# Performance work log

Measured on AMD Instinct MI355X. Metric: run time of the kernel, lower is better.

Reference implementation:

```python
import jax, jax.numpy as jnp
import numpy as np

N = 50000   # nodes
E = 1600000 # edges
D = 128     # feature dim (in = hidden = 128)


def setup_inputs() -> dict:
    key = jax.random.key(0)
    k1, k2, k3, k4 = jax.random.split(key, 4)
    scale = 1.0 / np.sqrt(D)
    return {
        "x": jax.random.normal(k1, (N, D), jnp.float32),
        "edge_index": jax.random.randint(k2, (2, E), 0, N, dtype=jnp.int32),
        "W0": jax.random.normal(k3, (D, D), jnp.float32) * scale,
        "b0": jnp.zeros((D,), jnp.float32),
        "W1": jax.random.normal(k4, (D, D), jnp.float32) * scale,
        "b1": jnp.zeros((D,), jnp.float32),
    }


def _gcn_norm(edge_index, num_nodes):
    # Add self-loops, compute symmetric normalization D^-1/2 A_hat D^-1/2.
    loop = jnp.arange(num_nodes, dtype=edge_index.dtype)
    src = jnp.concatenate([edge_index[0], loop])
    dst = jnp.concatenate([edge_index[1], loop])
    deg = jax.ops.segment_sum(jnp.ones_like(dst, jnp.float32), dst,
                              num_segments=num_nodes)
    dinv = jnp.where(deg > 0, jax.lax.rsqrt(deg), 0.0)
    norm = dinv[dst] * dinv[src]  # [E+N]
    return src, dst, norm


def _gcn_layer(x, src, dst, norm, W, b, num_nodes):
    h = x @ W                                  # [N, D]
    msg = h[src] * norm[:, None]               # gather + scale  [E+N, D]
    out = jax.ops.segment_sum(msg, dst, num_segments=num_nodes)  # scatter-add
    return out + b


def reference(x, edge_index, W0, b0, W1, b1):
    num_nodes = x.shape[0]
    src, dst, norm = _gcn_norm(edge_index, num_nodes)
    # forward loops over the first k=2 convs, ReLU after each (as in source)
    x = jax.nn.relu(_gcn_layer(x, src, dst, norm, W0, b0, num_nodes))
    x = jax.nn.relu(_gcn_layer(x, src, dst, norm, W1, b1, num_nodes))
    return x
```

## Files before the change

kernel.cpp:

```cpp
#include <hip/hip_runtime.h>
#include <hip/hip_bf16.h>

#define D 128
#define CHUNK 8192
#define SPAN_CAP 768


typedef __attribute__((ext_vector_type(8))) short short8;
typedef __attribute__((ext_vector_type(4))) float floatx4;

static __device__ inline unsigned int f2bf(float f) {
    unsigned int u = __float_as_uint(f);
    return (u + 0x7FFFu + ((u >> 16) & 1u)) >> 16;
}
static __device__ inline float bflo(unsigned int u) { return __uint_as_float(u << 16); }
static __device__ inline float bfhi(unsigned int u) { return __uint_as_float(u & 0xFFFF0000u); }

__global__ __launch_bounds__(256) void k01_swz_hist(const float* __restrict__ W0,
                                                    const float* __restrict__ W1,
                                                    short8* __restrict__ whi0, short8* __restrict__ wlo0,
                                                    short8* __restrict__ whi1, short8* __restrict__ wlo1,
                                                    const int* __restrict__ dst,
                                                    int* __restrict__ blockhist, int E_) {
    __shared__ int h[256];
    const int tid = threadIdx.x;
    if (blockIdx.x < 16) {
        int gid = blockIdx.x * 256 + tid;
        const float* W = (gid < 2048) ? W0 : W1;
        short8* whi = (gid < 2048) ? whi0 : whi1;
        short8* wlo = (gid < 2048) ? wlo0 : wlo1;
        int t2 = gid & 2047;
        int t = t2 >> 8, q = (t2 >> 6) & 3, lane = t2 & 63;
        short8 hi, lo;
        #pragma unroll
        for (int j = 0; j < 8; ++j) {
            int k = q * 32 + (lane >> 4) * 8 + j;
            int n = t * 16 + (lane & 15);
            float w = W[k * D + n];
            unsigned int hh = f2bf(w);
            hi[j] = (short)hh;
            lo[j] = (short)f2bf(w - __uint_as_float(hh << 16));
        }
        whi[t2] = hi;
        wlo[t2] = lo;
    } else {
        const int b = blockIdx.x - 16;
        h[tid] = 0;
        __syncthreads();
        const int e0 = b * CHUNK;
        const int e1 = min(E_, e0 + CHUNK);
        for (int e = e0 + tid; e < e1; e += 256)
            atomicAdd(&h[dst[e] >> 8], 1);
        __syncthreads();
        blockhist[b * 256 + tid] = h[tid];
    }
}

__global__ __launch_bounds__(256) void k23_scan_scatter(const int* __restrict__ blockhist,
                                                        const int* __restrict__ dst,
                                                        const int* __restrict__ src,
                                                        int* __restrict__ bucket_offs,
                                                        unsigned int* __restrict__ buf,
                                                        int NB, int NBUK, int E_) {
    __shared__ int s[256];
    __shared__ int c[256];
    const int myb = blockIdx.x, tid = threadIdx.x;
    int total = 0, prefix = 0;
    #pragma unroll 4
    for (int b2 = 0; b2 < NB; ++b2) {
        int t = blockhist[b2 * 256 + tid];
        total += t;
        prefix += (b2 < myb) ? t : 0;
    }
    s[tid] = total;
    __syncthreads();
    #pragma unroll
    for (int off = 1; off < 256; off <<= 1) {
        int x = (tid >= off) ? s[tid - off] : 0;
        __syncthreads();
        s[tid] += x;
        __syncthreads();
    }
    int bstart = s[tid] - total;
    if (myb == 0) {
        if (tid < NBUK) bucket_offs[tid] = bstart;
        if (tid == 0) bucket_offs[NBUK] = E_;
    }
    c[tid] = bstart + prefix;
    __syncthreads();

    const int e0 = myb * CHUNK;
    const int e1 = min(E_, e0 + CHUNK);
    for (int e = e0 + tid; e < e1; e += 256) {
        int v = dst[e];
        int sdx = src[e];
        int pos = atomicAdd(&c[v >> 8], 1);
        buf[pos] = (unsigned int)sdx | ((unsigned int)(v & 255) << 16);
    }
}

__global__ __launch_bounds__(256) void k4_bucket(const unsigned int* __restrict__ buf,
                                                 const int* __restrict__ bucket_offs,
                                                 int* __restrict__ offs,
                                                 float* __restrict__ dinv,
                                                 int* __restrict__ col, int N_, int E_) {
    __shared__ int h[256];
    __shared__ int s[256];
    __shared__ int c[256];
    const int beta = blockIdx.x, tid = threadIdx.x;
    const int start = bucket_offs[beta];
    const int end   = bucket_offs[beta + 1];

    h[tid] = 0;
    __syncthreads();
    for (int e = start + tid; e < end; e += 256)
        atomicAdd(&h[(buf[e] >> 16) & 255], 1);
    __syncthreads();

    int deg = h[tid];
    s[tid] = deg;
    __syncthreads();
    #pragma unroll
    for (int off = 1; off < 256; off <<= 1) {
        int x = (tid >= off) ? s[tid - off] : 0;
        __syncthreads();
        s[tid] += x;
        __syncthreads();
    }
    int excl = s[tid] - deg;

    int v0 = beta * 256 + tid;
    if (v0 < N_) {
        offs[v0] = start + excl;
        dinv[v0] = rsqrtf((float)(deg + 1));
    }
    if (beta == 0 && tid == 0) offs[N_] = E_;
    c[tid] = start + excl;
    __syncthreads();

    for (int e = start + tid; e < end; e += 256) {
        unsigned int p = buf[e];
        int pos = atomicAdd(&c[(p >> 16) & 255], 1);
        col[pos] = (int)(p & 0xFFFFu);
    }
}

__global__ __launch_bounds__(256) void gemm_mfma(const float* __restrict__ A,
                                                 const short8* __restrict__ whi,
                                                 const short8* __restrict__ wlo,
                                                 const float* __restrict__ dinv,
                                                 unsigned int* __restrict__ Gu, int nrows) {
    __shared__ float tileT[128][65];

    const int tid  = threadIdx.x;
    const int wave = tid >> 6, lane = tid & 63;
    const int m = lane & 15, quad = lane >> 4;
    const int rowInBlk = wave * 16;
    const int arow = min(blockIdx.x * 64 + rowInBlk + m, nrows - 1);
    const float* Ap = A + (size_t)arow * D + quad * 8;

    floatx4 acc[8];
    #pragma unroll
    for (int t = 0; t < 8; ++t) acc[t] = (floatx4){0.f, 0.f, 0.f, 0.f};

    #pragma unroll
    for (int q = 0; q < 4; ++q) {
        float4 a0 = *(const float4*)(Ap + q * 32);
        float4 a1 = *(const float4*)(Ap + q * 32 + 4);
        float av[8] = {a0.x, a0.y, a0.z, a0.w, a1.x, a1.y, a1.z, a1.w};
        short8 ahi, alo;
        #pragma unroll
        for (int j = 0; j < 8; ++j) {
            unsigned int h = f2bf(av[j]);
            ahi[j] = (short)h;
            alo[j] = (short)f2bf(av[j] - __uint_as_float(h << 16));
        }
        #pragma unroll
        for (int t = 0; t < 8; ++t) {
            short8 bh = whi[(t * 4 + q) * 64 + lane];
            short8 bl = wlo[(t * 4 + q) * 64 + lane];
            acc[t] = __builtin_amdgcn_mfma_f32_16x16x32_bf16(ahi, bh, acc[t], 0, 0, 0);
            acc[t] = __builtin_amdgcn_mfma_f32_16x16x32_bf16(alo, bh, acc[t], 0, 0, 0);
            acc[t] = __builtin_amdgcn_mfma_f32_16x16x32_bf16(ahi, bl, acc[t], 0, 0, 0);
        }
    }

    #pragma unroll
    for (int t = 0; t < 8; ++t)
        #pragma unroll
        for (int r = 0; r < 4; ++r)
            tileT[t * 16 + m][rowInBlk + quad * 4 + r] = acc[t][r];
    __syncthreads();

    const int orow = tid >> 2, seg = tid & 3;
    const int grow = blockIdx.x * 64 + orow;
    if (grow < nrows) {
        float s = dinv[grow];
        const int p = seg >> 1;
        unsigned int* Gp = Gu + ((size_t)(p * nrows + grow)) * 32 + (seg & 1) * 16;
        #pragma unroll
        for (int i = 0; i < 4; ++i) {
            int c0 = seg * 32 + i * 8;
            uint4 o4;
            o4.x = f2bf(tileT[c0 + 0][orow] * s) | (f2bf(tileT[c0 + 1][orow] * s) << 16);
            o4.y = f2bf(tileT[c0 + 2][orow] * s) | (f2bf(tileT[c0 + 3][orow] * s) << 16);
            o4.z = f2bf(tileT[c0 + 4][orow] * s) | (f2bf(tileT[c0 + 5][orow] * s) << 16);
            o4.w = f2bf(tileT[c0 + 6][orow] * s) | (f2bf(tileT[c0 + 7][orow] * s) << 16);
            ((uint4*)Gp)[i] = o4;
        }
    }
}

__global__ __launch_bounds__(256) void aggregate_kernel(const unsigned int* __restrict__ Gu,
                                                        const int* __restrict__ offs,
                                                        const int* __restrict__ col,
                                                        const float* __restrict__ dinv,
                                                        const float* __restrict__ bias,
                                                        float* __restrict__ out, int nnodes,
                                                        int ngroups) {
    __shared__ int scol[SPAN_CAP];
    __shared__ int soffs[9];
    const int bid   = blockIdx.x;
    const int xcd   = bid & 7;
    const int plane = xcd >> 2;
    const int i     = (bid >> 3) * 4 + (xcd & 3);
    if (i >= ngroups) return;
    const int tid   = threadIdx.x;
    const int node0 = i * 8;

    if (tid < 9) soffs[tid] = offs[min(node0 + tid, nnodes)];
    __syncthreads();
    const int s0   = soffs[0];
    const int span = soffs[8] - s0;
    const bool lds_ok = (span <= SPAN_CAP);
    if (lds_ok) {
        for (int k = tid; k < span; k += 256) scol[k] = col[s0 + k];
    }
    __syncthreads();

    const int lane = tid & 31;
    const int node = node0 + (tid >> 5);
    if (node >= nnodes) return;
    const unsigned int* P = Gu + (size_t)plane * nnodes * 32;

    unsigned int su = P[(size_t)node * 32 + lane];
    float ax = bflo(su), ay = bfhi(su);

    const int s = soffs[tid >> 5];
    const int e = soffs[(tid >> 5) + 1];
    int idx = s;

    if (lds_ok) {
        const int b0 = s - s0;
        int k = 0;
        const int deg = e - s;
        for (; k + 8 <= deg; k += 8) {
            int j0 = scol[b0 + k + 0], j1 = scol[b0 + k + 1], j2 = scol[b0 + k + 2], j3 = scol[b0 + k + 3];
            int j4 = scol[b0 + k + 4], j5 = scol[b0 + k + 5], j6 = scol[b0 + k + 6], j7 = scol[b0 + k + 7];
            unsigned int u0 = P[(size_t)j0 * 32 + lane];
            unsigned int u1 = P[(size_t)j1 * 32 + lane];
            unsigned int u2 = P[(size_t)j2 * 32 + lane];
            unsigned int u3 = P[(size_t)j3 * 32 + lane];
            unsigned int u4 = P[(size_t)j4 * 32 + lane];
            unsigned int u5 = P[(size_t)j5 * 32 + lane];
            unsigned int u6 = P[(size_t)j6 * 32 + lane];
            unsigned int u7 = P[(size_t)j7 * 32 + lane];
            ax += ((bflo(u0) + bflo(u1)) + (bflo(u2) + bflo(u3))) +
                  ((bflo(u4) + bflo(u5)) + (bflo(u6) + bflo(u7)));
            ay += ((bfhi(u0) + bfhi(u1)) + (bfhi(u2) + bfhi(u3))) +
                  ((bfhi(u4) + bfhi(u5)) + (bfhi(u6) + bfhi(u7)));
        }
        for (; k + 4 <= deg; k += 4) {
            int j0 = scol[b0 + k + 0], j1 = scol[b0 + k + 1], j2 = scol[b0 + k + 2], j3 = scol[b0 + k + 3];
            unsigned int u0 = P[(size_t)j0 * 32 + lane];
            unsigned int u1 = P[(size_t)j1 * 32 + lane];
            unsigned int u2 = P[(size_t)j2 * 32 + lane];
            unsigned int u3 = P[(size_t)j3 * 32 + lane];
            ax += (bflo(u0) + bflo(u1)) + (bflo(u2) + bflo(u3));
            ay += (bfhi(u0) + bfhi(u1)) + (bfhi(u2) + bfhi(u3));
        }
        for (; k < deg; ++k) {
            unsigned int u = P[(size_t)scol[b0 + k] * 32 + lane];
            ax += bflo(u);
            ay += bfhi(u);
        }
    } else {
        for (; idx + 4 <= e; idx += 4) {
            int j0 = col[idx + 0], j1 = col[idx + 1], j2 = col[idx + 2], j3 = col[idx + 3];
            unsigned int u0 = P[(size_t)j0 * 32 + lane];
            unsigned int u1 = P[(size_t)j1 * 32 + lane];
            unsigned int u2 = P[(size_t)j2 * 32 + lane];
            unsigned int u3 = P[(size_t)j3 * 32 + lane];
            ax += (bflo(u0) + bflo(u1)) + (bflo(u2) + bflo(u3));
            ay += (bfhi(u0) + bfhi(u1)) + (bfhi(u2) + bfhi(u3));
        }
        for (; idx < e; ++idx) {
            unsigned int u = P[(size_t)col[idx] * 32 + lane];
            ax += bflo(u);
            ay += bfhi(u);
        }
    }

    float dv = dinv[node];
    float2 bb = ((const float2*)bias)[plane * 32 + lane];
    float2 o;
    o.x = fmaxf(fmaf(dv, ax, bb.x), 0.f);
    o.y = fmaxf(fmaf(dv, ay, bb.y), 0.f);
    ((float2*)out)[(size_t)node * 64 + plane * 32 + lane] = o;
}

extern "C" void kernel_launch(void* const* d_in, const int* in_sizes, int n_in,
                              void* d_out, int out_size, void* d_ws, size_t ws_size,
                              hipStream_t stream) {
    const float* x    = (const float*)d_in[0];
    const int*   edge = (const int*)d_in[1];
    const float* W0   = (const float*)d_in[2];
    const float* b0   = (const float*)d_in[3];
    const float* W1   = (const float*)d_in[4];
    const float* b1   = (const float*)d_in[5];
    float* out = (float*)d_out;

    const int N_ = in_sizes[0] / D;
    const int E_ = in_sizes[1] / 2;
    const int* srcp = edge;
    const int* dstp = edge + E_;

    const int NB   = (E_ + CHUNK - 1) / CHUNK;
    const int NBUK = (N_ + 255) >> 8;

    char* p = (char*)d_ws;
    auto carve = [&](size_t bytes) { char* q = p; p += (bytes + 255) & ~(size_t)255; return q; };
    int*          blockhist = (int*)          carve((size_t)NB * 256 * 4);
    int*          buck_offs = (int*)          carve((size_t)(NBUK + 1) * 4);
    int*          offs      = (int*)          carve((size_t)(N_ + 1) * 4);
    float*        dinv      = (float*)        carve((size_t)N_ * 4);
    unsigned int* buf       = (unsigned int*) carve((size_t)E_ * 4);
    int*          col       = (int*)          carve((size_t)E_ * 4);
    unsigned int* gu        = (unsigned int*) carve((size_t)N_ * 64 * 4);
    short8*       whi0      = (short8*)       carve(2048 * 16);
    short8*       wlo0      = (short8*)       carve(2048 * 16);
    short8*       whi1      = (short8*)       carve(2048 * 16);
    short8*       wlo1      = (short8*)       carve(2048 * 16);

    k01_swz_hist   <<<16 + NB, 256, 0, stream>>>(W0, W1, whi0, wlo0, whi1, wlo1,
                                                 dstp, blockhist, E_);
    k23_scan_scatter<<<NB,     256, 0, stream>>>(blockhist, dstp, srcp, buck_offs, buf,
                                                 NB, NBUK, E_);
    k4_bucket      <<<NBUK,    256, 0, stream>>>(buf, buck_offs, offs, dinv, col, N_, E_);

    const int gmb = (N_ + 63) / 64;
    const int ngroups = (N_ + 7) / 8;
    const int agrid   = ((ngroups + 3) / 4) * 8;

    gemm_mfma       <<<gmb,   256, 0, stream>>>(x, whi0, wlo0, dinv, gu, N_);
    aggregate_kernel<<<agrid, 256, 0, stream>>>(gu, offs, col, dinv, b0, out, N_, ngroups);
    gemm_mfma       <<<gmb,   256, 0, stream>>>(out, whi1, wlo1, dinv, gu, N_);
    aggregate_kernel<<<agrid, 256, 0, stream>>>(gu, offs, col, dinv, b1, out, N_, ngroups);
}
```

Baseline: 258.7 us.

## Merge column planes into row-major gather table and drop XCD plane swizzle

Stores the bf16 projected features as full 256-byte rows instead of two 64-column planes, and has each aggregate block gather all 128 columns with 8-byte loads per lane. The XCD-based block remapping that pinned each plane to half the XCDs is removed, and the grid is halved. This cuts duplicate edge-index reads and the number of gather instructions, but each XCD's L2 now has to cache the whole feature table rather than half of it.

After: 268.7 us. 1.04x slower.

```diff
diff --git a/kernel.cpp b/kernel.cpp
--- a/kernel.cpp
+++ b/kernel.cpp
@@ -196,8 +196,7 @@
     const int grow = blockIdx.x * 64 + orow;
     if (grow < nrows) {
         float s = dinv[grow];
-        const int p = seg >> 1;
-        unsigned int* Gp = Gu + ((size_t)(p * nrows + grow)) * 32 + (seg & 1) * 16;
+        unsigned int* Gp = Gu + (size_t)grow * 64 + seg * 16;
         #pragma unroll
         for (int i = 0; i < 4; ++i) {
             int c0 = seg * 32 + i * 8;
@@ -216,17 +215,11 @@
                                                         const int* __restrict__ col,
                                                         const float* __restrict__ dinv,
                                                         const float* __restrict__ bias,
-                                                        float* __restrict__ out, int nnodes,
-                                                        int ngroups) {
+                                                        float* __restrict__ out, int nnodes) {
     __shared__ int scol[SPAN_CAP];
     __shared__ int soffs[9];
-    const int bid   = blockIdx.x;
-    const int xcd   = bid & 7;
-    const int plane = xcd >> 2;
-    const int i     = (bid >> 3) * 4 + (xcd & 3);
-    if (i >= ngroups) return;
     const int tid   = threadIdx.x;
-    const int node0 = i * 8;
+    const int node0 = blockIdx.x * 8;
 
     if (tid < 9) soffs[tid] = offs[min(node0 + tid, nnodes)];
     __syncthreads();
@@ -241,72 +234,89 @@
     const int lane = tid & 31;
     const int node = node0 + (tid >> 5);
     if (node >= nnodes) return;
-    const unsigned int* P = Gu + (size_t)plane * nnodes * 32;
-
-    unsigned int su = P[(size_t)node * 32 + lane];
-    float ax = bflo(su), ay = bfhi(su);
+
+    const unsigned int* Pl = Gu + 2 * lane;
+    #define LDROW(j) (*(const uint2*)(Pl + (size_t)(j) * 64))
+
+    uint2 su = LDROW(node);
+    float a0 = bflo(su.x), a1 = bfhi(su.x), a2 = bflo(su.y), a3 = bfhi(su.y);
 
     const int s = soffs[tid >> 5];
     const int e = soffs[(tid >> 5) + 1];
-    int idx = s;
 
     if (lds_ok) {
-        const int b0 = s - s0;
+        const int b0  = s - s0;
+        const int deg = e - s;
         int k = 0;
-        const int deg = e - s;
         for (; k + 8 <= deg; k += 8) {
             int j0 = scol[b0 + k + 0], j1 = scol[b0 + k + 1], j2 = scol[b0 + k + 2], j3 = scol[b0 + k + 3];
             int j4 = scol[b0 + k + 4], j5 = scol[b0 + k + 5], j6 = scol[b0 + k + 6], j7 = scol[b0 + k + 7];
-            unsigned int u0 = P[(size_t)j0 * 32 + lane];
-            unsigned int u1 = P[(size_t)j1 * 32 + lane];
-            unsigned int u2 = P[(size_t)j2 * 32 + lane];
-            unsigned int u3 = P[(size_t)j3 * 32 + lane];
-            unsigned int u4 = P[(size_t)j4 * 32 + lane];
-            unsigned int u5 = P[(size_t)j5 * 32 + lane];
-            unsigned int u6 = P[(size_t)j6 * 32 + lane];
-            unsigned int u7 = P[(size_t)j7 * 32 + lane];
-            ax += ((bflo(u0) + bflo(u1)) + (bflo(u2) + bflo(u3))) +
-                  ((bflo(u4) + bflo(u5)) + (bflo(u6) + bflo(u7)));
-            ay += ((bfhi(u0) + bfhi(u1)) + (bfhi(u2) + bfhi(u3))) +
-                  ((bfhi(u4) + bfhi(u5)) + (bfhi(u6) + bfhi(u7)));
+            uint2 u0 = LDROW(j0);
+            uint2 u1 = LDROW(j1);
+            uint2 u2 = LDROW(j2);
+            uint2 u3 = LDROW(j3);
+            uint2 u4 = LDROW(j4);
+            uint2 u5 = LDROW(j5);
+            uint2 u6 = LDROW(j6);
+            uint2 u7 = LDROW(j7);
+            a0 += ((bflo(u0.x) + bflo(u1.x)) + (bflo(u2.x) + bflo(u3.x))) +
+                  ((bflo(u4.x) + bflo(u5.x)) + (bflo(u6.x) + bflo(u7.x)));
+            a1 += ((bfhi(u0.x) + bfhi(u1.x)) + (bfhi(u2.x) + bfhi(u3.x))) +
+                  ((bfhi(u4.x) + bfhi(u5.x)) + (bfhi(u6.x) + bfhi(u7.x)));
+            a2 += ((bflo(u0.y) + bflo(u1.y)) + (bflo(u2.y) + bflo(u3.y))) +
+                  ((bflo(u4.y) + bflo(u5.y)) + (bflo(u6.y) + bflo(u7.y)));
+            a3 += ((bfhi(u0.y) + bfhi(u1.y)) + (bfhi(u2.y) + bfhi(u3.y))) +
+                  ((bfhi(u4.y) + bfhi(u5.y)) + (bfhi(u6.y) + bfhi(u7.y)));
         }
         for (; k + 4 <= deg; k += 4) {
             int j0 = scol[b0 + k + 0], j1 = scol[b0 + k + 1], j2 = scol[b0 + k + 2], j3 = scol[b0 + k + 3];
-            unsigned int u0 = P[(size_t)j0 * 32 + lane];
-            unsigned int u1 = P[(size_t)j1 * 32 + lane];
-            unsigned int u2 = P[(size_t)j2 * 32 + lane];
-            unsigned int u3 = P[(size_t)j3 * 32 + lane];
-            ax += (bflo(u0) + bflo(u1)) + (bflo(u2) + bflo(u3));
-            ay += (bfhi(u0) + bfhi(u1)) + (bfhi(u2) + bfhi(u3));
+            uint2 u0 = LDROW(j0);
+            uint2 u1 = LDROW(j1);
+            uint2 u2 = LDROW(j2);
+            uint2 u3 = LDROW(j3);
+            a0 += (bflo(u0.x) + bflo(u1.x)) + (bflo(u2.x) + bflo(u3.x));
+            a1 += (bfhi(u0.x) + bfhi(u1.x)) + (bfhi(u2.x) + bfhi(u3.x));
+            a2 += (bflo(u0.y) + bflo(u1.y)) + (bflo(u2.y) + bflo(u3.y));
+            a3 += (bfhi(u0.y) + bfhi(u1.y)) + (bfhi(u2.y) + bfhi(u3.y));
         }
         for (; k < deg; ++k) {
-            unsigned int u = P[(size_t)scol[b0 + k] * 32 + lane];
-            ax += bflo(u);
-            ay += bfhi(u);
+            uint2 u = LDROW(scol[b0 + k]);
+            a0 += bflo(u.x);
+            a1 += bfhi(u.x);
+            a2 += bflo(u.y);
+            a3 += bfhi(u.y);
         }
     } else {
+        int idx = s;
         for (; idx + 4 <= e; idx += 4) {
             int j0 = col[idx + 0], j1 = col[idx + 1], j2 = col[idx + 2], j3 = col[idx + 3];
-            unsigned int u0 = P[(size_t)j0 * 32 + lane];
-            unsigned int u1 = P[(size_t)j1 * 32 + lane];
-            unsigned int u2 = P[(size_t)j2 * 32 + lane];
-            unsigned int u3 = P[(size_t)j3 * 32 + lane];
-            ax += (bflo(u0) + bflo(u1)) + (bflo(u2) + bflo(u3));
-            ay += (bfhi(u0) + bfhi(u1)) + (bfhi(u2) + bfhi(u3));
+            uint2 u0 = LDROW(j0);
+            uint2 u1 = LDROW(j1);
+            uint2 u2 = LDROW(j2);
+            uint2 u3 = LDROW(j3);
+            a0 += (bflo(u0.x) + bflo(u1.x)) + (bflo(u2.x) + bflo(u3.x));
+            a1 += (bfhi(u0.x) + bfhi(u1.x)) + (bfhi(u2.x) + bfhi(u3.x));
+            a2 += (bflo(u0.y) + bflo(u1.y)) + (bflo(u2.y) + bflo(u3.y));
+            a3 += (bfhi(u0.y) + bfhi(u1.y)) + (bfhi(u2.y) + bfhi(u3.y));
         }
         for (; idx < e; ++idx) {
-            unsigned int u = P[(size_t)col[idx] * 32 + lane];
-            ax += bflo(u);
-            ay += bfhi(u);
-        }
-    }
+            uint2 u = LDROW(col[idx]);
+            a0 += bflo(u.x);
+            a1 += bfhi(u.x);
+            a2 += bflo(u.y);
+            a3 += bfhi(u.y);
+        }
+    }
+    #undef LDROW
 
     float dv = dinv[node];
-    float2 bb = ((const float2*)bias)[plane * 32 + lane];
-    float2 o;
-    o.x = fmaxf(fmaf(dv, ax, bb.x), 0.f);
-    o.y = fmaxf(fmaf(dv, ay, bb.y), 0.f);
-    ((float2*)out)[(size_t)node * 64 + plane * 32 + lane] = o;
+    float4 bb = ((const float4*)bias)[lane];
+    float4 o;
+    o.x = fmaxf(fmaf(dv, a0, bb.x), 0.f);
+    o.y = fmaxf(fmaf(dv, a1, bb.y), 0.f);
+    o.z = fmaxf(fmaf(dv, a2, bb.z), 0.f);
+    o.w = fmaxf(fmaf(dv, a3, bb.w), 0.f);
+    ((float4*)out)[(size_t)node * 32 + lane] = o;
 }
 
 extern "C" void kernel_launch(void* const* d_in, const int* in_sizes, int n_in,
@@ -348,12 +358,11 @@
                                                  NB, NBUK, E_);
     k4_bucket      <<<NBUK,    256, 0, stream>>>(buf, buck_offs, offs, dinv, col, N_, E_);
 
-    const int gmb = (N_ + 63) / 64;
+    const int gmb     = (N_ + 63) / 64;
     const int ngroups = (N_ + 7) / 8;
-    const int agrid   = ((ngroups + 3) / 4) * 8;
-
-    gemm_mfma       <<<gmb,   256, 0, stream>>>(x, whi0, wlo0, dinv, gu, N_);
-    aggregate_kernel<<<agrid, 256, 0, stream>>>(gu, offs, col, dinv, b0, out, N_, ngroups);
-    gemm_mfma       <<<gmb,   256, 0, stream>>>(out, whi1, wlo1, dinv, gu, N_);
-    aggregate_kernel<<<agrid, 256, 0, stream>>>(gu, offs, col, dinv, b1, out, N_, ngroups);
-}
+
+    gemm_mfma       <<<gmb,     256, 0, stream>>>(x, whi0, wlo0, dinv, gu, N_);
+    aggregate_kernel<<<ngroups, 256, 0, stream>>>(gu, offs, col, dinv, b0, out, N_);
+    gemm_mfma       <<<gmb,     256, 0, stream>>>(out, whi1, wlo1, dinv, gu, N_);
+    aggregate_kernel<<<ngroups, 256, 0, stream>>>(gu, offs, col, dinv, b1, out, N_);
+}
```

## Replace two-level bucket sort CSR build with global-atomic degree count and scatter

Applied to the files above, without the earlier changes.

Replaces the shared-memory two-pass bucket sort (block histograms, bucket scatter, per-bucket local sort) with a direct CSR build. Degrees come from global atomics, a two-kernel scan produces the offsets, and each edge is placed with an atomic on a per-node cursor. This removes the intermediate packed buffer and one full pass over the edges, but adds a memset, 1.6M global atomics spread over 50K nodes, and scattered writes. Column order within each row becomes nondeterministic, and the scan2 prefix only covers stot[0..63], so it supports at most 64K nodes.

After: 414.8 us. +60.4%, slower.

```diff
diff --git a/kernel.cpp b/kernel.cpp
--- a/kernel.cpp
+++ b/kernel.cpp
@@ -2,9 +2,7 @@
 #include <hip/hip_bf16.h>
 
 #define D 128
-#define CHUNK 8192
 #define SPAN_CAP 768
-
 
 typedef __attribute__((ext_vector_type(8))) short short8;
 typedef __attribute__((ext_vector_type(4))) float floatx4;
@@ -21,8 +19,7 @@
                                                     short8* __restrict__ whi0, short8* __restrict__ wlo0,
                                                     short8* __restrict__ whi1, short8* __restrict__ wlo1,
                                                     const int* __restrict__ dst,
-                                                    int* __restrict__ blockhist, int E_) {
-    __shared__ int h[256];
+                                                    int* __restrict__ deg, int E_) {
     const int tid = threadIdx.x;
     if (blockIdx.x < 16) {
         int gid = blockIdx.x * 256 + tid;
@@ -44,35 +41,25 @@
         whi[t2] = hi;
         wlo[t2] = lo;
     } else {
-        const int b = blockIdx.x - 16;
-        h[tid] = 0;
-        __syncthreads();
-        const int e0 = b * CHUNK;
-        const int e1 = min(E_, e0 + CHUNK);
-        for (int e = e0 + tid; e < e1; e += 256)
-            atomicAdd(&h[dst[e] >> 8], 1);
-        __syncthreads();
-        blockhist[b * 256 + tid] = h[tid];
-    }
-}
-
-__global__ __launch_bounds__(256) void k23_scan_scatter(const int* __restrict__ blockhist,
-                                                        const int* __restrict__ dst,
-                                                        const int* __restrict__ src,
-                                                        int* __restrict__ bucket_offs,
-                                                        unsigned int* __restrict__ buf,
-                                                        int NB, int NBUK, int E_) {
+        const int nb = gridDim.x - 16;
+        const int b  = blockIdx.x - 16;
+        for (int e = b * 256 + tid; e < E_; e += nb * 256)
+            atomicAdd(&deg[dst[e]], 1);
+    }
+}
+
+__global__ __launch_bounds__(256) void scan1(const int* __restrict__ deg,
+                                             int* __restrict__ tmp,
+                                             int* __restrict__ stot, int N_) {
     __shared__ int s[256];
-    __shared__ int c[256];
-    const int myb = blockIdx.x, tid = threadIdx.x;
-    int total = 0, prefix = 0;
-    #pragma unroll 4
-    for (int b2 = 0; b2 < NB; ++b2) {
-        int t = blockhist[b2 * 256 + tid];
-        total += t;
-        prefix += (b2 < myb) ? t : 0;
-    }
-    s[tid] = total;
+    const int b = blockIdx.x, tid = threadIdx.x;
+    const int base = b * 1024 + tid * 4;
+    int d0 = (base + 0 < N_) ? deg[base + 0] : 0;
+    int d1 = (base + 1 < N_) ? deg[base + 1] : 0;
+    int d2 = (base + 2 < N_) ? deg[base + 2] : 0;
+    int d3 = (base + 3 < N_) ? deg[base + 3] : 0;
+    int tsum = d0 + d1 + d2 + d3;
+    s[tid] = tsum;
     __syncthreads();
     #pragma unroll
     for (int off = 1; off < 256; off <<= 1) {
@@ -81,67 +68,54 @@
         s[tid] += x;
         __syncthreads();
     }
-    int bstart = s[tid] - total;
-    if (myb == 0) {
-        if (tid < NBUK) bucket_offs[tid] = bstart;
-        if (tid == 0) bucket_offs[NBUK] = E_;
-    }
-    c[tid] = bstart + prefix;
-    __syncthreads();
-
-    const int e0 = myb * CHUNK;
-    const int e1 = min(E_, e0 + CHUNK);
-    for (int e = e0 + tid; e < e1; e += 256) {
-        int v = dst[e];
-        int sdx = src[e];
-        int pos = atomicAdd(&c[v >> 8], 1);
-        buf[pos] = (unsigned int)sdx | ((unsigned int)(v & 255) << 16);
-    }
-}
-
-__global__ __launch_bounds__(256) void k4_bucket(const unsigned int* __restrict__ buf,
-                                                 const int* __restrict__ bucket_offs,
-                                                 int* __restrict__ offs,
-                                                 float* __restrict__ dinv,
-                                                 int* __restrict__ col, int N_, int E_) {
-    __shared__ int h[256];
-    __shared__ int s[256];
-    __shared__ int c[256];
-    const int beta = blockIdx.x, tid = threadIdx.x;
-    const int start = bucket_offs[beta];
-    const int end   = bucket_offs[beta + 1];
-
-    h[tid] = 0;
-    __syncthreads();
-    for (int e = start + tid; e < end; e += 256)
-        atomicAdd(&h[(buf[e] >> 16) & 255], 1);
-    __syncthreads();
-
-    int deg = h[tid];
-    s[tid] = deg;
-    __syncthreads();
-    #pragma unroll
-    for (int off = 1; off < 256; off <<= 1) {
-        int x = (tid >= off) ? s[tid - off] : 0;
-        __syncthreads();
-        s[tid] += x;
-        __syncthreads();
-    }
-    int excl = s[tid] - deg;
-
-    int v0 = beta * 256 + tid;
-    if (v0 < N_) {
-        offs[v0] = start + excl;
-        dinv[v0] = rsqrtf((float)(deg + 1));
-    }
-    if (beta == 0 && tid == 0) offs[N_] = E_;
-    c[tid] = start + excl;
-    __syncthreads();
-
-    for (int e = start + tid; e < end; e += 256) {
-        unsigned int p = buf[e];
-        int pos = atomicAdd(&c[(p >> 16) & 255], 1);
-        col[pos] = (int)(p & 0xFFFFu);
+    int excl = s[tid] - tsum;
+    if (base + 0 < N_) tmp[base + 0] = excl;
+    if (base + 1 < N_) tmp[base + 1] = excl + d0;
+    if (base + 2 < N_) tmp[base + 2] = excl + d0 + d1;
+    if (base + 3 < N_) tmp[base + 3] = excl + d0 + d1 + d2;
+    if (tid == 255) stot[b] = s[255];
+}
+
+__global__ __launch_bounds__(256) void scan2(const int* __restrict__ deg,
+                                             const int* __restrict__ tmp,
+                                             const int* __restrict__ stot,
+                                             int* __restrict__ offs,
+                                             int* __restrict__ cursor,
+                                             float* __restrict__ dinv,
+                                             int N_, int E_) {
+    __shared__ int sbase;
+    const int b = blockIdx.x, tid = threadIdx.x;
+    if (tid < 64) {
+        int v = (tid < b) ? stot[tid] : 0;
+        #pragma unroll
+        for (int off = 32; off > 0; off >>= 1) v += __shfl_down(v, off);
+        if (tid == 0) sbase = v;
+    }
+    __syncthreads();
+    const int base = sbase;
+    const int i = b * 1024 + tid * 4;
+    #pragma unroll
+    for (int k = 0; k < 4; ++k) {
+        if (i + k < N_) {
+            int o = tmp[i + k] + base;
+            offs[i + k]   = o;
+            cursor[i + k] = o;
+            dinv[i + k]   = rsqrtf((float)(deg[i + k] + 1));
+        }
+    }
+    if (b == 0 && tid == 0) offs[N_] = E_;
+}
+
+__global__ __launch_bounds__(256) void k_scatter(const int* __restrict__ dst,
+                                                 const int* __restrict__ src,
+                                                 int* __restrict__ cursor,
+                                                 int* __restrict__ col, int E_) {
+    const int stride = gridDim.x * 256;
+    for (int e = blockIdx.x * 256 + threadIdx.x; e < E_; e += stride) {
+        int d = dst[e];
+        int s = src[e];
+        int pos = atomicAdd(&cursor[d], 1);
+        col[pos] = s;
     }
 }
 
@@ -325,28 +299,30 @@
     const int* srcp = edge;
     const int* dstp = edge + E_;
 
-    const int NB   = (E_ + CHUNK - 1) / CHUNK;
-    const int NBUK = (N_ + 255) >> 8;
-
     char* p = (char*)d_ws;
     auto carve = [&](size_t bytes) { char* q = p; p += (bytes + 255) & ~(size_t)255; return q; };
-    int*          blockhist = (int*)          carve((size_t)NB * 256 * 4);
-    int*          buck_offs = (int*)          carve((size_t)(NBUK + 1) * 4);
-    int*          offs      = (int*)          carve((size_t)(N_ + 1) * 4);
-    float*        dinv      = (float*)        carve((size_t)N_ * 4);
-    unsigned int* buf       = (unsigned int*) carve((size_t)E_ * 4);
-    int*          col       = (int*)          carve((size_t)E_ * 4);
-    unsigned int* gu        = (unsigned int*) carve((size_t)N_ * 64 * 4);
-    short8*       whi0      = (short8*)       carve(2048 * 16);
-    short8*       wlo0      = (short8*)       carve(2048 * 16);
-    short8*       whi1      = (short8*)       carve(2048 * 16);
-    short8*       wlo1      = (short8*)       carve(2048 * 16);
-
-    k01_swz_hist   <<<16 + NB, 256, 0, stream>>>(W0, W1, whi0, wlo0, whi1, wlo1,
-                                                 dstp, blockhist, E_);
-    k23_scan_scatter<<<NB,     256, 0, stream>>>(blockhist, dstp, srcp, buck_offs, buf,
-                                                 NB, NBUK, E_);
-    k4_bucket      <<<NBUK,    256, 0, stream>>>(buf, buck_offs, offs, dinv, col, N_, E_);
+    int*          deg     = (int*)          carve((size_t)N_ * 4);
+    int*          tmp     = (int*)          carve((size_t)N_ * 4);
+    int*          stot    = (int*)          carve(64 * 4);
+    int*          offs    = (int*)          carve((size_t)(N_ + 1) * 4);
+    int*          cursor  = (int*)          carve((size_t)N_ * 4);
+    float*        dinv    = (float*)        carve((size_t)N_ * 4);
+    int*          col     = (int*)          carve((size_t)E_ * 4);
+    unsigned int* gu      = (unsigned int*) carve((size_t)N_ * 64 * 4);
+    short8*       whi0    = (short8*)       carve(2048 * 16);
+    short8*       wlo0    = (short8*)       carve(2048 * 16);
+    short8*       whi1    = (short8*)       carve(2048 * 16);
+    short8*       wlo1    = (short8*)       carve(2048 * 16);
+
+    const int NS1 = (N_ + 1023) / 1024;
+    const int sgrid = min((E_ + 255) / 256, 2048);
+
+    hipMemsetAsync(deg, 0, (size_t)N_ * 4, stream);
+    k01_swz_hist<<<16 + 240, 256, 0, stream>>>(W0, W1, whi0, wlo0, whi1, wlo1,
+                                               dstp, deg, E_);
+    scan1       <<<NS1,   256, 0, stream>>>(deg, tmp, stot, N_);
+    scan2       <<<NS1,   256, 0, stream>>>(deg, tmp, stot, offs, cursor, dinv, N_, E_);
+    k_scatter   <<<sgrid, 256, 0, stream>>>(dstp, srcp, cursor, col, E_);
 
     const int gmb = (N_ + 63) / 64;
     const int ngroups = (N_ + 7) / 8;
```

## Replace per-block histogram scan with global atomic bucket reservation in CSR build

Applied to the files above, without the earlier changes.

The counting-sort CSR build no longer stores a per-block histogram that every scatter block must rescan. Blocks now atomically accumulate a single global 256-bucket histogram, a one-block kernel scans it, and scatter blocks re-histogram their chunk and reserve ranges through atomic cursors. The chunk size shrinks to launch more blocks, and the per-bucket kernel grows to 1024 threads to spread each bucket's work. This adds an extra launch, a memset, a second pass over dst per chunk, and makes the order of edges within a bucket nondeterministic. The code assumes at most 256 buckets.

After: 269.1 us. +4.0%, slower.

```diff
diff --git a/kernel.cpp b/kernel.cpp
--- a/kernel.cpp
+++ b/kernel.cpp
@@ -2,7 +2,7 @@
 #include <hip/hip_bf16.h>
 
 #define D 128
-#define CHUNK 8192
+#define CHUNK 2048
 #define SPAN_CAP 768
 
 
@@ -21,7 +21,7 @@
                                                     short8* __restrict__ whi0, short8* __restrict__ wlo0,
                                                     short8* __restrict__ whi1, short8* __restrict__ wlo1,
                                                     const int* __restrict__ dst,
-                                                    int* __restrict__ blockhist, int E_) {
+                                                    int* __restrict__ bhist, int E_) {
     __shared__ int h[256];
     const int tid = threadIdx.x;
     if (blockIdx.x < 16) {
@@ -52,27 +52,19 @@
         for (int e = e0 + tid; e < e1; e += 256)
             atomicAdd(&h[dst[e] >> 8], 1);
         __syncthreads();
-        blockhist[b * 256 + tid] = h[tid];
-    }
-}
-
-__global__ __launch_bounds__(256) void k23_scan_scatter(const int* __restrict__ blockhist,
-                                                        const int* __restrict__ dst,
-                                                        const int* __restrict__ src,
-                                                        int* __restrict__ bucket_offs,
-                                                        unsigned int* __restrict__ buf,
-                                                        int NB, int NBUK, int E_) {
+        int c = h[tid];
+        if (c) atomicAdd(&bhist[tid], c);
+    }
+}
+
+__global__ __launch_bounds__(256) void k_scan_buckets(const int* __restrict__ bhist,
+                                                      int* __restrict__ bucket_offs,
+                                                      int* __restrict__ gcursor,
+                                                      int NBUK, int E_) {
     __shared__ int s[256];
-    __shared__ int c[256];
-    const int myb = blockIdx.x, tid = threadIdx.x;
-    int total = 0, prefix = 0;
-    #pragma unroll 4
-    for (int b2 = 0; b2 < NB; ++b2) {
-        int t = blockhist[b2 * 256 + tid];
-        total += t;
-        prefix += (b2 < myb) ? t : 0;
-    }
-    s[tid] = total;
+    const int tid = threadIdx.x;
+    int t = bhist[tid];
+    s[tid] = t;
     __syncthreads();
     #pragma unroll
     for (int off = 1; off < 256; off <<= 1) {
@@ -81,29 +73,47 @@
         s[tid] += x;
         __syncthreads();
     }
-    int bstart = s[tid] - total;
-    if (myb == 0) {
-        if (tid < NBUK) bucket_offs[tid] = bstart;
-        if (tid == 0) bucket_offs[NBUK] = E_;
-    }
-    c[tid] = bstart + prefix;
-    __syncthreads();
-
-    const int e0 = myb * CHUNK;
+    int excl = s[tid] - t;
+    bucket_offs[tid] = excl;
+    gcursor[tid]     = excl;
+    if (tid == 0) bucket_offs[256] = E_;
+}
+
+__global__ __launch_bounds__(256) void k_scatter_resv(const int* __restrict__ dst,
+                                                      const int* __restrict__ src,
+                                                      int* __restrict__ gcursor,
+                                                      unsigned int* __restrict__ buf, int E_) {
+    __shared__ int h[256];
+    __shared__ int base[256];
+    const int b = blockIdx.x, tid = threadIdx.x;
+    const int e0 = b * CHUNK;
     const int e1 = min(E_, e0 + CHUNK);
+
+    h[tid] = 0;
+    __syncthreads();
+    for (int e = e0 + tid; e < e1; e += 256)
+        atomicAdd(&h[dst[e] >> 8], 1);
+    __syncthreads();
+    int cnt = h[tid];
+    if (cnt) base[tid] = atomicAdd(&gcursor[tid], cnt);
+    __syncthreads();
+    h[tid] = 0;
+    __syncthreads();
+
     for (int e = e0 + tid; e < e1; e += 256) {
         int v = dst[e];
         int sdx = src[e];
-        int pos = atomicAdd(&c[v >> 8], 1);
+        int beta = v >> 8;
+        int pos = base[beta] + atomicAdd(&h[beta], 1);
         buf[pos] = (unsigned int)sdx | ((unsigned int)(v & 255) << 16);
     }
 }
 
-__global__ __launch_bounds__(256) void k4_bucket(const unsigned int* __restrict__ buf,
-                                                 const int* __restrict__ bucket_offs,
-                                                 int* __restrict__ offs,
-                                                 float* __restrict__ dinv,
-                                                 int* __restrict__ col, int N_, int E_) {
+__global__ __launch_bounds__(1024) void k4_bucket(const unsigned int* __restrict__ buf,
+                                                  const int* __restrict__ bucket_offs,
+                                                  int* __restrict__ offs,
+                                                  float* __restrict__ dinv,
+                                                  int* __restrict__ col, int N_, int E_) {
     __shared__ int h[256];
     __shared__ int s[256];
     __shared__ int c[256];
@@ -111,34 +121,35 @@
     const int start = bucket_offs[beta];
     const int end   = bucket_offs[beta + 1];
 
-    h[tid] = 0;
-    __syncthreads();
-    for (int e = start + tid; e < end; e += 256)
+    if (tid < 256) h[tid] = 0;
+    __syncthreads();
+    for (int e = start + tid; e < end; e += 1024)
         atomicAdd(&h[(buf[e] >> 16) & 255], 1);
     __syncthreads();
 
-    int deg = h[tid];
-    s[tid] = deg;
+    int deg = (tid < 256) ? h[tid] : 0;
+    if (tid < 256) s[tid] = deg;
     __syncthreads();
     #pragma unroll
     for (int off = 1; off < 256; off <<= 1) {
-        int x = (tid >= off) ? s[tid - off] : 0;
-        __syncthreads();
-        s[tid] += x;
-        __syncthreads();
-    }
-    int excl = s[tid] - deg;
-
-    int v0 = beta * 256 + tid;
-    if (v0 < N_) {
-        offs[v0] = start + excl;
-        dinv[v0] = rsqrtf((float)(deg + 1));
+        int x = (tid >= off && tid < 256) ? s[tid - off] : 0;
+        __syncthreads();
+        if (tid < 256) s[tid] += x;
+        __syncthreads();
+    }
+    if (tid < 256) {
+        int excl = s[tid] - deg;
+        int v0 = beta * 256 + tid;
+        if (v0 < N_) {
+            offs[v0] = start + excl;
+            dinv[v0] = rsqrtf((float)(deg + 1));
+        }
+        c[tid] = start + excl;
     }
     if (beta == 0 && tid == 0) offs[N_] = E_;
-    c[tid] = start + excl;
-    __syncthreads();
-
-    for (int e = start + tid; e < end; e += 256) {
+    __syncthreads();
+
+    for (int e = start + tid; e < end; e += 1024) {
         unsigned int p = buf[e];
         int pos = atomicAdd(&c[(p >> 16) & 255], 1);
         col[pos] = (int)(p & 0xFFFFu);
@@ -330,8 +341,9 @@
 
     char* p = (char*)d_ws;
     auto carve = [&](size_t bytes) { char* q = p; p += (bytes + 255) & ~(size_t)255; return q; };
-    int*          blockhist = (int*)          carve((size_t)NB * 256 * 4);
-    int*          buck_offs = (int*)          carve((size_t)(NBUK + 1) * 4);
+    int*          bhist     = (int*)          carve(256 * 4);
+    int*          buck_offs = (int*)          carve(257 * 4);
+    int*          gcursor   = (int*)          carve(256 * 4);
     int*          offs      = (int*)          carve((size_t)(N_ + 1) * 4);
     float*        dinv      = (float*)        carve((size_t)N_ * 4);
     unsigned int* buf       = (unsigned int*) carve((size_t)E_ * 4);
@@ -342,11 +354,12 @@
     short8*       whi1      = (short8*)       carve(2048 * 16);
     short8*       wlo1      = (short8*)       carve(2048 * 16);
 
-    k01_swz_hist   <<<16 + NB, 256, 0, stream>>>(W0, W1, whi0, wlo0, whi1, wlo1,
-                                                 dstp, blockhist, E_);
-    k23_scan_scatter<<<NB,     256, 0, stream>>>(blockhist, dstp, srcp, buck_offs, buf,
-                                                 NB, NBUK, E_);
-    k4_bucket      <<<NBUK,    256, 0, stream>>>(buf, buck_offs, offs, dinv, col, N_, E_);
+    hipMemsetAsync(bhist, 0, 256 * 4, stream);
+    k01_swz_hist  <<<16 + NB, 256,  0, stream>>>(W0, W1, whi0, wlo0, whi1, wlo1,
+                                                 dstp, bhist, E_);
+    k_scan_buckets<<<1,       256,  0, stream>>>(bhist, buck_offs, gcursor, NBUK, E_);
+    k_scatter_resv<<<NB,      256,  0, stream>>>(dstp, srcp, gcursor, buf, E_);
+    k4_bucket     <<<NBUK,    1024, 0, stream>>>(buf, buck_offs, offs, dinv, col, N_, E_);
 
     const int gmb = (N_ + 63) / 64;
     const int ngroups = (N_ + 7) / 8;
```
